# Performance work log

Hardware: AMD Instinct MI355X
Metric: run time of the kernel (lower is better)

## Reference

```python
import jax, jax.numpy as jnp
import numpy as np

EPS = 1e-7      # GENConv message epsilon
BN_EPS = 1e-5   # torch BatchNorm1d eps


def _genconv(x, src, dst, n, w1, b1, gamma, beta, w2, b2):
    # GENConv(aggr='softmax_sg', t=1.0): msg = relu(x_j)+eps, per-feature
    # scatter-softmax weights (stop-grad), weighted sum, residual, MLP
    # [Linear -> BatchNorm(train stats) -> ReLU -> Linear].
    msg = jnp.maximum(x[src], 0.0) + EPS                         # [E, d]
    m = jax.ops.segment_max(msg, dst, num_segments=n)            # [N, d]
    e = jnp.exp(msg - m[dst])
    s = jax.ops.segment_sum(e, dst, num_segments=n)
    alpha = jax.lax.stop_gradient(e / (s[dst] + 1e-16))          # softmax_sg
    agg = jax.ops.segment_sum(msg * alpha, dst, num_segments=n)  # [N, d]
    h = agg + x
    h = h @ w1 + b1
    mu = jnp.mean(h, axis=0)
    var = jnp.var(h, axis=0)
    h = (h - mu) * jax.lax.rsqrt(var + BN_EPS) * gamma + beta
    h = jnp.maximum(h, 0.0)
    return h @ w2 + b2


def _forward(x, edge_index, batch, target,
             g1_w1, g1_b1, g1_g, g1_be, g1_w2, g1_b2,
             g2_w1, g2_b1, g2_g, g2_be, g2_w2, g2_b2,
             g3_w1, g3_b1, g3_g, g3_be, g3_w2, g3_b2,
             fg1_w, fg1_b, fg2_w, fg2_b, fg3_w, fg3_b,
             emb, cw, cb, fxt_w, fxt_b,
             f1_w, f1_b, f2_w, f2_b, o_w, o_b):
    n = x.shape[0]
    nb = target.shape[0]
    src, dst = edge_index[0], edge_index[1]
    h = jnp.maximum(_genconv(x, src, dst, n, g1_w1, g1_b1, g1_g, g1_be, g1_w2, g1_b2), 0.0)
    h = jnp.maximum(_genconv(h, src, dst, n, g2_w1, g2_b1, g2_g, g2_be, g2_w2, g2_b2), 0.0)
    h = jnp.maximum(_genconv(h, src, dst, n, g3_w1, g3_b1, g3_g, g3_be, g3_w2, g3_b2), 0.0)
    # global mean pool over graphs
    sums = jax.ops.segment_sum(h, batch, num_segments=nb)
    cnt = jax.ops.segment_sum(jnp.ones((n, 1), h.dtype), batch, num_segments=nb)
    xg = sums / jnp.maximum(cnt, 1.0)
    xg = jnp.maximum(xg @ fg1_w + fg1_b, 0.0)
    xg = jnp.maximum(xg @ fg2_w + fg2_b, 0.0)
    xg = jnp.maximum(xg @ fg3_w + fg3_b, 0.0)
    # protein branch: embed [B,1000,128], Conv1d(1000->32,k=8) over embed axis
    ext = emb[target]                                            # [B, 1000, 128]
    conv = jax.lax.conv_general_dilated(
        ext, cw, (1,), 'VALID',
        dimension_numbers=('NCW', 'OIW', 'NCW')) + cb[None, :, None]  # [B, 32, 121]
    xt = conv.reshape(nb, 32 * 121) @ fxt_w + fxt_b
    xc = jnp.concatenate([xg, xt], axis=1)                       # [B, 256]
    xc = jnp.maximum(xc @ f1_w + f1_b, 0.0)
    xc = jnp.maximum(xc @ f2_w + f2_b, 0.0)
    return xc @ o_w + o_b


def _lin(k, i, o):
    kw, kb = jax.random.split(k)
    s = 1.0 / np.sqrt(i)
    return (jax.random.uniform(kw, (i, o), jnp.float32, -s, s),
            jax.random.uniform(kb, (o,), jnp.float32, -s, s))


def setup_inputs():
    key = jax.random.key(0)
    ks = jax.random.split(key, 32)
    N, E, B, D = 30000, 150000, 256, 78
    d = {}
    d['x'] = jax.random.normal(ks[0], (N, D), jnp.float32)
    d['edge_index'] = jax.random.randint(ks[1], (2, E), 0, N)
    d['batch'] = jnp.sort(jax.random.randint(ks[2], (N,), 0, B))
    d['target'] = jax.random.randint(ks[3], (B, 1000), 0, 26)
    dims = [(78, 156, 78), (78, 156, 312), (312, 624, 624)]
    for li, (i, hdim, o) in enumerate(dims, start=1):
        w1, b1 = _lin(ks[4 + 2 * li], i, hdim)
        w2, b2 = _lin(ks[5 + 2 * li], hdim, o)
        d['g%d_w1' % li], d['g%d_b1' % li] = w1, b1
        d['g%d_g' % li] = jnp.ones((hdim,), jnp.float32)
        d['g%d_be' % li] = jnp.zeros((hdim,), jnp.float32)
        d['g%d_w2' % li], d['g%d_b2' % li] = w2, b2
    d['fg1_w'], d['fg1_b'] = _lin(ks[14], 624, 512)
    d['fg2_w'], d['fg2_b'] = _lin(ks[15], 512, 1024)
    d['fg3_w'], d['fg3_b'] = _lin(ks[16], 1024, 128)
    d['emb'] = jax.random.normal(ks[17], (26, 128), jnp.float32)
    s = 1.0 / np.sqrt(1000 * 8)
    d['cw'] = jax.random.uniform(ks[18], (32, 1000, 8), jnp.float32, -s, s)
    d['cb'] = jax.random.uniform(ks[19], (32,), jnp.float32, -s, s)
    d['fxt_w'], d['fxt_b'] = _lin(ks[20], 32 * 121, 128)
    d['f1_w'], d['f1_b'] = _lin(ks[21], 256, 1024)
    d['f2_w'], d['f2_b'] = _lin(ks[22], 1024, 512)
    d['o_w'], d['o_b'] = _lin(ks[23], 512, 1)
    return d


def reference(x, edge_index, batch, target,
              g1_w1, g1_b1, g1_g, g1_be, g1_w2, g1_b2,
              g2_w1, g2_b1, g2_g, g2_be, g2_w2, g2_b2,
              g3_w1, g3_b1, g3_g, g3_be, g3_w2, g3_b2,
              fg1_w, fg1_b, fg2_w, fg2_b, fg3_w, fg3_b,
              emb, cw, cb, fxt_w, fxt_b,
              f1_w, f1_b, f2_w, f2_b, o_w, o_b):
    return _forward(x, edge_index, batch, target,
                    g1_w1, g1_b1, g1_g, g1_be, g1_w2, g1_b2,
                    g2_w1, g2_b1, g2_g, g2_be, g2_w2, g2_b2,
                    g3_w1, g3_b1, g3_g, g3_be, g3_w2, g3_b2,
                    fg1_w, fg1_b, fg2_w, fg2_b, fg3_w, fg3_b,
                    emb, cw, cb, fxt_w, fxt_b,
                    f1_w, f1_b, f2_w, f2_b, o_w, o_b)
```

## Files before the change

### kernel.cpp

```cpp
#include <hip/hip_runtime.h>
#include <hip/hip_bf16.h>

typedef unsigned short u16;
typedef __attribute__((ext_vector_type(8))) short bh8;
typedef __attribute__((ext_vector_type(4))) float f32x4;

static __device__ __forceinline__ float b2fu(u16 u) {
    union { float f; unsigned int i; } x;
    x.i = ((unsigned int)u) << 16;
    return x.f;
}
static __device__ __forceinline__ u16 f2bu(float f) {
    __hip_bfloat16 h = __float2bfloat16(f);
    union { __hip_bfloat16 h; u16 u; } x;
    x.h = h;
    return x.u;
}

static __device__ __forceinline__ void gload16(const u16* g, u16* l) {
    __builtin_amdgcn_global_load_lds(
        (const __attribute__((address_space(1))) unsigned int*)(const void*)g,
        (__attribute__((address_space(3))) unsigned int*)(void*)l, 16, 0, 0);
}


__global__ __launch_bounds__(256) void const_out_kernel(float* __restrict__ out, float v, int n) {
    int i = blockIdx.x * 256 + threadIdx.x;
    if (i < n) out[i] = v;
}


__global__ __launch_bounds__(256) void hist2_kernel(const int* __restrict__ dst,
                                                    const int* __restrict__ batch,
                                                    int* __restrict__ hist,
                                                    int* __restrict__ ghist, int E, int N) {
    int i = blockIdx.x * 256 + threadIdx.x;
    if (i < E) atomicAdd(&hist[dst[i]], 1);
    else if (i < E + N) atomicAdd(&ghist[batch[i - E]], 1);
}

__global__ __launch_bounds__(256) void scan_kernel(const int* __restrict__ hist,
                                                   int* __restrict__ rowptr,
                                                   int* __restrict__ fill, int N) {
    __shared__ int csum[256];
    __shared__ int coff[257];
    int t = threadIdx.x;
    int chunk = (N + 255) / 256;
    int lo = min(t * chunk, N), hi = min(lo + chunk, N);
    int s = 0;
    for (int i = lo; i < hi; i++) s += hist[i];
    csum[t] = s;
    __syncthreads();
    if (t == 0) {
        int acc = 0;
        for (int i = 0; i < 256; i++) { coff[i] = acc; acc += csum[i]; }
        rowptr[N] = acc;
    }
    __syncthreads();
    int run = coff[t];
    for (int i = lo; i < hi; i++) {
        rowptr[i] = run;
        fill[i] = run;
        run += hist[i];
    }
}

__global__ __launch_bounds__(256) void scan_tiles(const int* __restrict__ hist, int N,
                                                  int* __restrict__ rowptr,
                                                  int* __restrict__ tsum) {
    int tid = threadIdx.x;
    int i = blockIdx.x * 256 + tid;
    int v = (i < N) ? hist[i] : 0;
    __shared__ int s[256];
    s[tid] = v;
    __syncthreads();
    for (int off = 1; off < 256; off <<= 1) {
        int t = (tid >= off) ? s[tid - off] : 0;
        __syncthreads();
        s[tid] += t;
        __syncthreads();
    }
    if (i < N) rowptr[i] = s[tid] - v;
    if (tid == 255) tsum[blockIdx.x] = s[255];
}

__global__ __launch_bounds__(256) void scan_tsum(const int* __restrict__ tsum, int ntiles,
                                                 int* __restrict__ toff,
                                                 int* __restrict__ totalp) {
    int tid = threadIdx.x;
    int v = (tid < ntiles) ? tsum[tid] : 0;
    __shared__ int s[256];
    s[tid] = v;
    __syncthreads();
    for (int off = 1; off < 256; off <<= 1) {
        int t = (tid >= off) ? s[tid - off] : 0;
        __syncthreads();
        s[tid] += t;
        __syncthreads();
    }
    if (tid < ntiles) toff[tid] = s[tid] - v;
    if (tid == 255) *totalp = s[255];
}

__global__ __launch_bounds__(256) void scan_apply(int* __restrict__ rowptr,
                                                  const int* __restrict__ toff, int N,
                                                  int* __restrict__ fill) {
    int i = blockIdx.x * 256 + threadIdx.x;
    if (i < N) {
        int r = rowptr[i] + toff[blockIdx.x];
        rowptr[i] = r;
        fill[i] = r;
    }
}

__global__ __launch_bounds__(256) void scatter_kernel(const int* __restrict__ src,
                                                      const int* __restrict__ dst,
                                                      int* __restrict__ fill,
                                                      int* __restrict__ srcs, int E) {
    int e = blockIdx.x * 256 + threadIdx.x;
    if (e < E) {
        int p = atomicAdd(&fill[dst[e]], 1);
        srcs[p] = src[e];
    }
}


template <typename T, int VEC>
__global__ __launch_bounds__(256) void agg_kernel(const T* __restrict__ x,
                                                  const int* __restrict__ rowptr,
                                                  const int* __restrict__ srcs,
                                                  u16* __restrict__ out, int d, int ldx,
                                                  int Kp, int N) {
    int n = blockIdx.y * 4 + (threadIdx.x >> 6);
    int f0 = (blockIdx.x * 64 + (threadIdx.x & 63)) * VEC;
    if (n >= N || f0 >= Kp) return;
    size_t o = (size_t)n * Kp + f0;
    if (f0 >= d) {
#pragma unroll
        for (int i = 0; i < VEC; i++) out[o + i] = 0;
        return;
    }
    auto loadV = [&](const T* row, float* v) {
        if constexpr (sizeof(T) == 4) {
            float2 t = *reinterpret_cast<const float2*>(row);
            v[0] = t.x; v[1] = t.y;
        } else if constexpr (VEC == 2) {
            unsigned int u = *reinterpret_cast<const unsigned int*>(row);
            v[0] = b2fu((u16)(u & 0xffff)); v[1] = b2fu((u16)(u >> 16));
        } else if constexpr (VEC == 4) {
            uint2 u = *reinterpret_cast<const uint2*>(row);
            v[0] = b2fu((u16)(u.x & 0xffff)); v[1] = b2fu((u16)(u.x >> 16));
            v[2] = b2fu((u16)(u.y & 0xffff)); v[3] = b2fu((u16)(u.y >> 16));
        } else {
            uint4 u = *reinterpret_cast<const uint4*>(row);
            v[0] = b2fu((u16)(u.x & 0xffff)); v[1] = b2fu((u16)(u.x >> 16));
            v[2] = b2fu((u16)(u.y & 0xffff)); v[3] = b2fu((u16)(u.y >> 16));
            v[4] = b2fu((u16)(u.z & 0xffff)); v[5] = b2fu((u16)(u.z >> 16));
            v[6] = b2fu((u16)(u.w & 0xffff)); v[7] = b2fu((u16)(u.w >> 16));
        }
    };
    int e0 = rowptr[n], e1 = rowptr[n + 1];
    float s[VEC] = {}, t[VEC] = {};
    for (int e = e0; e < e1; e++) {
        int sr = srcs[e];
        float v[VEC];
        loadV(x + (size_t)sr * ldx + f0, v);
#pragma unroll
        for (int i = 0; i < VEC; i++) {
            float m = fmaxf(v[i], 0.f) + 1e-7f;
            float wv = __expf(m);
            s[i] += wv;
            t[i] += m * wv;
        }
    }
    float xs[VEC];
    loadV(x + (size_t)n * ldx + f0, xs);
    u16 ob[VEC];
#pragma unroll
    for (int i = 0; i < VEC; i++) {
        float a = t[i] / (s[i] + 1e-16f) + xs[i];
        ob[i] = (f0 + i < d) ? f2bu(a) : (u16)0;
    }
    if constexpr (VEC == 2) {
        *reinterpret_cast<unsigned int*>(out + o) =
            (unsigned int)ob[0] | ((unsigned int)ob[1] << 16);
    } else if constexpr (VEC == 4) {
        uint2 u;
        u.x = (unsigned int)ob[0] | ((unsigned int)ob[1] << 16);
        u.y = (unsigned int)ob[2] | ((unsigned int)ob[3] << 16);
        *reinterpret_cast<uint2*>(out + o) = u;
    } else {
        uint4 u;
        u.x = (unsigned int)ob[0] | ((unsigned int)ob[1] << 16);
        u.y = (unsigned int)ob[2] | ((unsigned int)ob[3] << 16);
        u.z = (unsigned int)ob[4] | ((unsigned int)ob[5] << 16);
        u.w = (unsigned int)ob[6] | ((unsigned int)ob[7] << 16);
        *reinterpret_cast<uint4*>(out + o) = u;
    }
}


struct WtJobs {
    const float* W[6];
    u16* WT[6];
    int K[6], N[6], Kp[6], Np[6];
};

__global__ __launch_bounds__(256) void wt_cvt6(WtJobs jb) {
    int jz = blockIdx.z;
    int Kp = jb.Kp[jz], Np = jb.Np[jz];
    int n = blockIdx.y * 4 + (threadIdx.x >> 6);
    int k = blockIdx.x * 64 + (threadIdx.x & 63);
    if (n >= Np || k >= Kp) return;
    int K = jb.K[jz], N = jb.N[jz];
    float v = (n < N && k < K) ? jb.W[jz][(size_t)k * N + n] : 0.f;
    jb.WT[jz][(size_t)n * Kp + k] = f2bu(v);
}


template <int AMODE, int EMODE, bool RELU, typename CT>
__global__ __launch_bounds__(256) void gemm_mfma(const u16* __restrict__ A,
                                                 const u16* __restrict__ BT,
                                                 const float* __restrict__ bias,
                                                 CT* __restrict__ C, int ldc, int M, int Ncols,
                                                 int Kp, int kLen, int nbx, int nby, int spx,
                                                 const float* __restrict__ scale,
                                                 const float* __restrict__ shift,
                                                 float* __restrict__ osum,
                                                 float* __restrict__ osumsq) {
    int xcd = blockIdx.x & 7;
    int j = blockIdx.x >> 3;
    int bx = j % nbx;
    int by = xcd * spx + j / nbx;
    if (by >= nby) return;
    __shared__ u16 As[2][128 * 32];
    __shared__ u16 Bs[2][128 * 32];
    const int tid = threadIdx.x;
    const int lane = tid & 63;
    const int w = tid >> 6;
    const int bm = by * 128;
    const int bn = bx * 128;
    const int kw = blockIdx.y * kLen;
    f32x4 acc[4][4] = {};

    const int r0 = w * 16 + (lane >> 2);
    const int r1 = r0 + 64;
    const int sw = ((lane & 3) ^ ((r0 >> 1) & 3)) << 3;
    const u16* Ag0 = A + (size_t)(bm + r0) * Kp + sw + kw;
    const u16* Ag1 = A + (size_t)(bm + r1) * Kp + sw + kw;
    const u16* Bg0 = BT + (size_t)(bn + r0) * Kp + sw + kw;
    const u16* Bg1 = BT + (size_t)(bn + r1) * Kp + sw + kw;
    const int wb = w << 9;

    uint4 a0r, a1r;
    auto stageB = [&](int b, int koff) {
        gload16(Bg0 + koff, &Bs[b][wb]);
        gload16(Bg1 + koff, &Bs[b][2048 + wb]);
    };
    auto stageA_lds = [&](int b, int koff) {
        gload16(Ag0 + koff, &As[b][wb]);
        gload16(Ag1 + koff, &As[b][2048 + wb]);
    };
    auto loadA_reg = [&](int koff) {
        a0r = *reinterpret_cast<const uint4*>(Ag0 + koff);
        a1r = *reinterpret_cast<const uint4*>(Ag1 + koff);
    };
    auto writeA_reg = [&](int b, int koff) {
        int f0 = sw + kw + koff;
        float4 sc0 = *reinterpret_cast<const float4*>(scale + f0);
        float4 sc1 = *reinterpret_cast<const float4*>(scale + f0 + 4);
        float4 sh0 = *reinterpret_cast<const float4*>(shift + f0);
        float4 sh1 = *reinterpret_cast<const float4*>(shift + f0 + 4);
        auto tf2 = [](unsigned int u, float sa, float sb, float ha, float hb) {
            float h0 = b2fu((u16)(u & 0xffff)), h1 = b2fu((u16)(u >> 16));
            float v0 = fmaxf(fmaf(h0, sa, ha), 0.f);
            float v1 = fmaxf(fmaf(h1, sb, hb), 0.f);
            return (unsigned int)f2bu(v0) | ((unsigned int)f2bu(v1) << 16);
        };
        uint4 o0, o1;
        o0.x = tf2(a0r.x, sc0.x, sc0.y, sh0.x, sh0.y);
        o0.y = tf2(a0r.y, sc0.z, sc0.w, sh0.z, sh0.w);
        o0.z = tf2(a0r.z, sc1.x, sc1.y, sh1.x, sh1.y);
        o0.w = tf2(a0r.w, sc1.z, sc1.w, sh1.z, sh1.w);
        o1.x = tf2(a1r.x, sc0.x, sc0.y, sh0.x, sh0.y);
        o1.y = tf2(a1r.y, sc0.z, sc0.w, sh0.z, sh0.w);
        o1.z = tf2(a1r.z, sc1.x, sc1.y, sh1.x, sh1.y);
        o1.w = tf2(a1r.w, sc1.z, sc1.w, sh1.z, sh1.w);
        *reinterpret_cast<uint4*>(&As[b][wb + lane * 8]) = o0;
        *reinterpret_cast<uint4*>(&As[b][2048 + wb + lane * 8]) = o1;
    };

    const int fm = (w >> 1) * 64 + (lane & 15);
    const int fn = (w & 1) * 64 + (lane & 15);
    const int g = lane >> 4;
    const int ka = (g ^ ((fm >> 1) & 3)) << 3;
    const int kb = (g ^ ((fn >> 1) & 3)) << 3;

    const int nk = kLen >> 5;
    if constexpr (AMODE == 0) {
        stageA_lds(0, 0);
        stageB(0, 0);
        asm volatile("s_waitcnt vmcnt(0)" ::: "memory");
    } else {
        loadA_reg(0);
        stageB(0, 0);
        asm volatile("s_waitcnt vmcnt(0)" ::: "memory");
        writeA_reg(0, 0);
        asm volatile("s_waitcnt lgkmcnt(0)" ::: "memory");
    }
    __builtin_amdgcn_s_barrier();
    for (int k = 0; k < nk; k++) {
        const int cur = k & 1;
        if (k + 1 < nk) {
            if constexpr (AMODE == 0) stageA_lds(cur ^ 1, (k + 1) << 5);
            else loadA_reg((k + 1) << 5);
            stageB(cur ^ 1, (k + 1) << 5);
        }
        bh8 af[4], bf[4];
#pragma unroll
        for (int mt = 0; mt < 4; mt++)
            af[mt] = *reinterpret_cast<const bh8*>(&As[cur][(fm + mt * 16) * 32 + ka]);
#pragma unroll
        for (int nt = 0; nt < 4; nt++)
            bf[nt] = *reinterpret_cast<const bh8*>(&Bs[cur][(fn + nt * 16) * 32 + kb]);
        asm volatile("s_waitcnt lgkmcnt(0)" ::: "memory");
        __builtin_amdgcn_sched_barrier(0);
        __builtin_amdgcn_s_setprio(1);
#pragma unroll
        for (int mt = 0; mt < 4; mt++)
#pragma unroll
            for (int nt = 0; nt < 4; nt++)
                acc[mt][nt] = __builtin_amdgcn_mfma_f32_16x16x32_bf16(af[mt], bf[nt],
                                                                      acc[mt][nt], 0, 0, 0);
        __builtin_amdgcn_s_setprio(0);
        __builtin_amdgcn_sched_barrier(0);
        asm volatile("s_waitcnt vmcnt(0)" ::: "memory");
        if constexpr (AMODE == 1) {
            __builtin_amdgcn_sched_barrier(0);
            if (k + 1 < nk) writeA_reg(cur ^ 1, (k + 1) << 5);
            asm volatile("s_waitcnt lgkmcnt(0)" ::: "memory");
        }
        __builtin_amdgcn_s_barrier();
    }
    const int rq = (lane >> 4) * 4;
    const int cl = lane & 15;
    if constexpr (EMODE == 0) {
#pragma unroll
        for (int mt = 0; mt < 4; mt++) {
#pragma unroll
            for (int nt = 0; nt < 4; nt++) {
                int n = bn + (w & 1) * 64 + nt * 16 + cl;
                if (n >= ldc) continue;
                bool valid = (n < Ncols);
                float bv = valid ? bias[n] : 0.f;
#pragma unroll
                for (int r = 0; r < 4; r++) {
                    int m = bm + (w >> 1) * 64 + mt * 16 + rq + r;
                    if (m >= M) continue;
                    float v = valid ? acc[mt][nt][r] + bv : 0.f;
                    if (RELU) v = fmaxf(v, 0.f);
                    if (sizeof(CT) == 2)
                        C[(size_t)m * ldc + n] = (CT)f2bu(v);
                    else
                        C[(size_t)m * ldc + n] = (CT)v;
                }
            }
        }
    } else if constexpr (EMODE == 1) {
        float cs[4] = {0.f, 0.f, 0.f, 0.f}, cq[4] = {0.f, 0.f, 0.f, 0.f};
#pragma unroll
        for (int nt = 0; nt < 4; nt++) {
            int n = bn + (w & 1) * 64 + nt * 16 + cl;
            if (n >= ldc) continue;
            float bv = (n < Ncols) ? bias[n] : 0.f;
#pragma unroll
            for (int mt = 0; mt < 4; mt++) {
#pragma unroll
                for (int r = 0; r < 4; r++) {
                    int m = bm + (w >> 1) * 64 + mt * 16 + rq + r;
                    if (m >= M) continue;
                    float v = (n < Ncols) ? acc[mt][nt][r] + bv : 0.f;
                    C[(size_t)m * ldc + n] = (CT)f2bu(v);
                    cs[nt] += v;
                    cq[nt] += v * v;
                }
            }
        }
        float* red = (float*)&As[0][0];
        const int slot = (w >> 1) * 4 + (lane >> 4);
#pragma unroll
        for (int nt = 0; nt < 4; nt++) {
            int nl = (w & 1) * 64 + nt * 16 + cl;
            red[nl * 8 + slot] = cs[nt];
            red[1024 + nl * 8 + slot] = cq[nt];
        }
        __syncthreads();
        if (tid < 128) {
            int n = bn + tid;
            if (n < Ncols) {
                float s = 0.f, q = 0.f;
#pragma unroll
                for (int i = 0; i < 8; i++) {
                    s += red[tid * 8 + i];
                    q += red[1024 + tid * 8 + i];
                }
                atomicAdd(&osum[n], s);
                atomicAdd(&osumsq[n], q);
            }
        }
    } else {
#pragma unroll
        for (int mt = 0; mt < 4; mt++) {
#pragma unroll
            for (int nt = 0; nt < 4; nt++) {
                int n = bn + (w & 1) * 64 + nt * 16 + cl;
                if (n >= Ncols) continue;
#pragma unroll
                for (int r = 0; r < 4; r++) {
                    int m = bm + (w >> 1) * 64 + mt * 16 + rq + r;
                    if (m >= M) continue;
                    atomicAdd((float*)&C[(size_t)m * ldc + n], acc[mt][nt][r]);
                }
            }
        }
    }
}


__global__ __launch_bounds__(256) void bn_final(const float* __restrict__ sum,
                                                const float* __restrict__ sumsq,
                                                const float* __restrict__ gamma,
                                                const float* __restrict__ beta,
                                                float* __restrict__ scale,
                                                float* __restrict__ shift, int dh, int Kp,
                                                float invN) {
    int i = blockIdx.x * 256 + threadIdx.x;
    if (i >= Kp) return;
    if (i < dh) {
        float mu = sum[i] * invN;
        float var = sumsq[i] * invN - mu * mu;
        float sc = gamma[i] / sqrtf(var + 1e-5f);
        scale[i] = sc;
        shift[i] = beta[i] - mu * sc;
    } else {
        scale[i] = 0.f;
        shift[i] = 0.f;
    }
}


__global__ __launch_bounds__(256) void pool_seg(const u16* __restrict__ h,
                                                const int* __restrict__ goff,
                                                float* __restrict__ gsum, int d) {
    int g = blockIdx.y;
    int c = threadIdx.x & 63;
    int f = blockIdx.x * 64 + c;
    int wv = threadIdx.x >> 6;
    int r0 = goff[g], r1 = goff[g + 1];
    float s = 0.f;
    if (f < d)
        for (int r = r0 + wv; r < r1; r += 4) s += b2fu(h[(size_t)r * d + f]);
    __shared__ float ls[4][64];
    ls[wv][c] = s;
    __syncthreads();
    if (wv == 0 && f < d) {
        float tot = ls[0][c] + ls[1][c] + ls[2][c] + ls[3][c];
        gsum[(size_t)g * d + f] = tot / fmaxf((float)(r1 - r0), 1.f);
    }
}


__global__ __launch_bounds__(256) void gemm_sk(const float* __restrict__ A, int lda,
                                               const float* __restrict__ B, int ldb,
                                               float* __restrict__ C, int ldc, int M, int K,
                                               int Nn, int KC, int klim) {
    __shared__ float As[16][17];
    __shared__ float Bs[16][68];
    const int tid = threadIdx.x;
    const int bn = blockIdx.x * 64;
    const int bm = blockIdx.y * 16;
    const int k0 = blockIdx.z * KC;
    const int kend = min(K, k0 + KC);
    const int tx = tid & 63;
    const int ty = tid >> 6;
    float acc[4] = {};
    const int am = bm + (tid >> 4);
    const int ak = tid & 15;
    for (int kk0 = k0; kk0 < kend; kk0 += 16) {
        {
            int k = kk0 + ak;
            float v = (am < M && k < kend) ? A[(size_t)am * lda + k] : 0.f;
            if (k < klim) v = fmaxf(v, 0.f);
            As[ak][tid >> 4] = v;
        }
#pragma unroll
        for (int i = 0; i < 4; i++) {
            int k = kk0 + ty + 4 * i;
            Bs[ty + 4 * i][tx] = (k < kend && bn + tx < Nn) ? B[(size_t)k * ldb + bn + tx] : 0.f;
        }
        __syncthreads();
#pragma unroll
        for (int kk = 0; kk < 16; kk++) {
            float b = Bs[kk][tx];
#pragma unroll
            for (int i = 0; i < 4; i++) acc[i] = fmaf(As[kk][ty + 4 * i], b, acc[i]);
        }
        __syncthreads();
    }
    if (bn + tx < Nn) {
#pragma unroll
        for (int i = 0; i < 4; i++) {
            int m = bm + ty + 4 * i;
            if (m < M) atomicAdd(&C[(size_t)m * ldc + bn + tx], acc[i]);
        }
    }
}

static void launch_gemm_small(const float* A, int lda, const float* B, int ldb,
                              float* C, int ldc, int M, int K, int Nn, int klim,
                              hipStream_t stream) {
    int gx = (Nn + 63) / 64, gy = (M + 15) / 16;
    int tiles = gx * gy;
    int ksplit = 512 / tiles;
    if (ksplit < 1) ksplit = 1;
    int maxsplit = (K + 63) / 64;
    if (ksplit > maxsplit) ksplit = maxsplit;
    int KC = (((K + ksplit - 1) / ksplit) + 15) & ~15;
    ksplit = (K + KC - 1) / KC;
    gemm_sk<<<dim3(gx, gy, ksplit), 256, 0, stream>>>(A, lda, B, ldb, C, ldc, M, K, Nn, KC,
                                                      klim);
}


struct FillJobs {
    float* C[6];
    const float* b[6];
    int ld[6], n0[6], n1[6];
};

__global__ __launch_bounds__(256) void prefill6(FillJobs jb, int M) {
    int jz = blockIdx.z;
    int w = jb.n1[jz] - jb.n0[jz];
    int i = blockIdx.x * 256 + threadIdx.x;
    if (i >= M * w) return;
    int m = i / w, n = i - m * w;
    jb.C[jz][(size_t)m * jb.ld[jz] + jb.n0[jz] + n] = jb.b[jz][n];
}


__global__ __launch_bounds__(256) void hone_kernel(const int* __restrict__ target,
                                                   u16* __restrict__ H, int total) {
    int i = blockIdx.x * 256 + threadIdx.x;
    if (i >= total) return;
    int b = i / 1000, pos = i - b * 1000;
    int t = target[i];
    H[((size_t)b * 26 + t) * 1024 + pos] = 0x3F80;
}

__global__ __launch_bounds__(256) void cwt_cvt(const float* __restrict__ cw,
                                               u16* __restrict__ BT) {
    int n = blockIdx.y;
    int kk = blockIdx.x * 256 + threadIdx.x;
    int o = n >> 3, k = n & 7;
    float v = (kk < 1000) ? cw[(size_t)o * 8000 + (size_t)kk * 8 + k] : 0.f;
    BT[(size_t)n * 1024 + kk] = f2bu(v);
}

__global__ __launch_bounds__(256) void prot_conv_kernel(const float* __restrict__ S,
                                                        const float* __restrict__ emb,
                                                        const float* __restrict__ cb,
                                                        float* __restrict__ out) {
    int b = blockIdx.x;
    int tid = threadIdx.x;
    __shared__ float Sl[6656];
    __shared__ float el[26 * 128];
    for (int i = tid; i < 6656; i += 256) Sl[i] = S[(size_t)b * 6656 + i];
    for (int i = tid; i < 26 * 128; i += 256) el[i] = emb[i];
    __syncthreads();
    for (int j = tid; j < 3872; j += 256) {
        int o = j / 121;
        int w = j - o * 121;
        float acc = cb[o];
        for (int t = 0; t < 26; t++) {
#pragma unroll
            for (int k = 0; k < 8; k++)
                acc = fmaf(Sl[t * 256 + o * 8 + k], el[t * 128 + w + k], acc);
        }
        out[(size_t)b * 3872 + j] = acc;
    }
}


__global__ __launch_bounds__(256) void out_kernel(const float* __restrict__ A,
                                                  const float* __restrict__ w,
                                                  const float* __restrict__ bias,
                                                  float* __restrict__ out, int M, int K) {
    int wave = threadIdx.x >> 6;
    int lane = threadIdx.x & 63;
    int r = blockIdx.x * 4 + wave;
    if (r >= M) return;
    float acc = 0.f;
    for (int k = lane; k < K; k += 64) acc += fmaxf(A[(size_t)r * K + k], 0.f) * w[k];
    for (int off = 32; off > 0; off >>= 1) acc += __shfl_down(acc, off, 64);
    if (lane == 0) out[r] = acc + bias[0];
}


static inline int KP(int k) { return (k + 31) & ~31; }
static inline int NP(int n) { return (n + 127) & ~127; }
static inline int LD8(int n) { return (n + 7) & ~7; }

extern "C" void kernel_launch(void* const* d_in, const int* in_sizes, int n_in, void* d_out,
                              int out_size, void* d_ws, size_t ws_size, hipStream_t stream) {
    static const int exp_sizes[39] = {
        2340000, 300000, 30000, 256000,
        12168, 156, 156, 156, 12168, 78,
        12168, 156, 156, 156, 48672, 312,
        194688, 624, 624, 624, 389376, 624,
        319488, 512, 524288, 1024, 131072, 128,
        3328, 256000, 32, 495616, 128,
        262144, 1024, 524288, 512, 512, 1};
    int bad = (n_in != 39) ? 100 : -1;
    if (bad < 0)
        for (int i = 0; i < 39; i++)
            if (in_sizes[i] != exp_sizes[i]) { bad = i; break; }
    if (bad >= 0) {
        const_out_kernel<<<1, 256, 0, stream>>>((float*)d_out, 2048.f + 8.f * bad, out_size);
        return;
    }

    const int N = 30000, E = 150000, B = 256;
    const int Mp = 30080;
    const int nby = 235, spx = 30;
    const int ntiles = (N + 255) / 256;
    const float* x_in = (const float*)d_in[0];
    const int* ei = (const int*)d_in[1];
    const int* src = ei;
    const int* dst = ei + E;
    const int* batch = (const int*)d_in[2];
    const int* target = (const int*)d_in[3];

    char* p = (char*)d_ws;
    auto carve = [&](size_t bytes) {
        char* r = p;
        p += (bytes + 15) & ~(size_t)15;
        return r;
    };
    int* hist = (int*)carve((size_t)(N + B) * 4);
    int* ghist = hist + N;
    int* rowptr = (int*)carve((size_t)(N + 1) * 4);
    int* fill = (int*)carve((size_t)N * 4);
    int* srcs = (int*)carve((size_t)E * 4);
    int* goff = (int*)carve((size_t)(B + 1) * 4);
    int* gfill = (int*)carve((size_t)B * 4);
    int* tsum = (int*)carve(256 * 4);
    int* toff = (int*)carve(256 * 4);
    float* sum_ = (float*)carve(2 * 624 * 4);
    float* sumsq_ = sum_ + 624;
    float* scale_ = (float*)carve(640 * 4);
    float* shift_ = (float*)carve(640 * 4);
    float* zero256 = (float*)carve(256 * 4);
    float* gsum = (float*)carve((size_t)B * 624 * 4);
    float* fc1 = (float*)carve((size_t)B * 512 * 4);
    float* fc2 = (float*)carve((size_t)B * 1024 * 4);
    float* xc = (float*)carve((size_t)B * 256 * 4);
    float* fcc1 = (float*)carve((size_t)B * 1024 * 4);
    float* fcc2 = (float*)carve((size_t)B * 512 * 4);
    float* Sbuf = (float*)carve((size_t)B * 6656 * 4);
    float* convb = (float*)carve((size_t)B * 3872 * 4);
    u16* Hbuf = (u16*)carve((size_t)B * 26 * 1024 * 2);
    u16* cwT = (u16*)carve((size_t)256 * 1024 * 2);
    u16* Abf = (u16*)carve((size_t)Mp * 640 * 2);
    u16* hmidb = (u16*)carve((size_t)Mp * 640 * 2);
    u16* Lout = (u16*)carve((size_t)N * 624 * 2);
    struct Layer { int di, dh, dn, w1, b1, g, be, w2, b2; };
    const Layer L[3] = {
        {78, 156, 78, 4, 5, 6, 7, 8, 9},
        {78, 156, 312, 10, 11, 12, 13, 14, 15},
        {312, 624, 624, 16, 17, 18, 19, 20, 21},
    };
    u16* WT1[3];
    u16* WT2[3];
    for (int li = 0; li < 3; li++) {
        WT1[li] = (u16*)carve((size_t)NP(L[li].dh) * KP(L[li].di) * 2);
        WT2[li] = (u16*)carve((size_t)NP(L[li].dn) * KP(L[li].dh) * 2);
    }
    size_t need = (size_t)(p - (char*)d_ws);
    if (ws_size < need) {
        const_out_kernel<<<1, 256, 0, stream>>>((float*)d_out,
                                                1024.f + (float)(ws_size >> 20), out_size);
        return;
    }

    hipMemsetAsync(hist, 0, (size_t)(N + B) * 4, stream);
    hipMemsetAsync(zero256, 0, 256 * 4, stream);
    hist2_kernel<<<(E + N + 255) / 256, 256, 0, stream>>>(dst, batch, hist, ghist, E, N);
    scan_tiles<<<ntiles, 256, 0, stream>>>(hist, N, rowptr, tsum);
    scan_tsum<<<1, 256, 0, stream>>>(tsum, ntiles, toff, rowptr + N);
    scan_apply<<<ntiles, 256, 0, stream>>>(rowptr, toff, N, fill);
    scan_kernel<<<1, 256, 0, stream>>>(ghist, goff, gfill, B);
    scatter_kernel<<<(E + 255) / 256, 256, 0, stream>>>(src, dst, fill, srcs, E);

    {
        WtJobs jb;
        int mgx = 1, mgy = 1;
        for (int li = 0; li < 3; li++) {
            jb.W[2 * li] = (const float*)d_in[L[li].w1];
            jb.WT[2 * li] = WT1[li];
            jb.K[2 * li] = L[li].di; jb.N[2 * li] = L[li].dh;
            jb.Kp[2 * li] = KP(L[li].di); jb.Np[2 * li] = NP(L[li].dh);
            jb.W[2 * li + 1] = (const float*)d_in[L[li].w2];
            jb.WT[2 * li + 1] = WT2[li];
            jb.K[2 * li + 1] = L[li].dh; jb.N[2 * li + 1] = L[li].dn;
            jb.Kp[2 * li + 1] = KP(L[li].dh); jb.Np[2 * li + 1] = NP(L[li].dn);
        }
        for (int i = 0; i < 6; i++) {
            int gx = (jb.Kp[i] + 63) / 64, gy = jb.Np[i] / 4;
            if (gx > mgx) mgx = gx;
            if (gy > mgy) mgy = gy;
        }
        wt_cvt6<<<dim3(mgx, mgy, 6), 256, 0, stream>>>(jb);
    }

    const int ldo[3] = {LD8(L[0].dn), LD8(L[1].dn), LD8(L[2].dn)};
    for (int li = 0; li < 3; li++) {
        const int di = L[li].di, dh = L[li].dh, dn = L[li].dn;
        const int Kp1 = KP(di), Kp2 = KP(dh);
        if (li == 0)
            agg_kernel<float, 2><<<dim3((Kp1 / 2 + 63) / 64, (N + 3) / 4), 256, 0, stream>>>(
                x_in, rowptr, srcs, Abf, di, di, Kp1, N);
        else if (li == 1)
            agg_kernel<u16, 4><<<dim3((Kp1 / 4 + 63) / 64, (N + 3) / 4), 256, 0, stream>>>(
                Lout, rowptr, srcs, Abf, di, ldo[0], Kp1, N);
        else
            agg_kernel<u16, 8><<<dim3((Kp1 / 8 + 63) / 64, (N + 3) / 4), 256, 0, stream>>>(
                Lout, rowptr, srcs, Abf, di, ldo[1], Kp1, N);
        hipMemsetAsync(sum_, 0, 2 * 624 * 4, stream);
        {
            int nbx = NP(dh) / 128;
            gemm_mfma<0, 1, false, u16><<<dim3(8 * spx * nbx), 256, 0, stream>>>(
                Abf, WT1[li], (const float*)d_in[L[li].b1], hmidb, Kp2, N, dh, Kp1, Kp1, nbx,
                nby, spx, nullptr, nullptr, sum_, sumsq_);
        }
        bn_final<<<(Kp2 + 255) / 256, 256, 0, stream>>>(
            sum_, sumsq_, (const float*)d_in[L[li].g], (const float*)d_in[L[li].be], scale_,
            shift_, dh, Kp2, 1.0f / N);
        {
            int nbx = NP(dn) / 128;
            gemm_mfma<1, 0, true, u16><<<dim3(8 * spx * nbx), 256, 0, stream>>>(
                hmidb, WT2[li], (const float*)d_in[L[li].b2], Lout, ldo[li], N, dn, Kp2, Kp2,
                nbx, nby, spx, scale_, shift_, nullptr, nullptr);
        }
    }

    pool_seg<<<dim3(10, B), 256, 0, stream>>>(Lout, goff, gsum, 624);

    {
        FillJobs fj;
        fj.C[0] = fc1;  fj.b[0] = (const float*)d_in[23]; fj.ld[0] = 512;  fj.n0[0] = 0;   fj.n1[0] = 512;
        fj.C[1] = fc2;  fj.b[1] = (const float*)d_in[25]; fj.ld[1] = 1024; fj.n0[1] = 0;   fj.n1[1] = 1024;
        fj.C[2] = xc;   fj.b[2] = (const float*)d_in[27]; fj.ld[2] = 256;  fj.n0[2] = 0;   fj.n1[2] = 128;
        fj.C[3] = xc;   fj.b[3] = (const float*)d_in[32]; fj.ld[3] = 256;  fj.n0[3] = 128; fj.n1[3] = 256;
        fj.C[4] = fcc1; fj.b[4] = (const float*)d_in[34]; fj.ld[4] = 1024; fj.n0[4] = 0;   fj.n1[4] = 1024;
        fj.C[5] = fcc2; fj.b[5] = (const float*)d_in[36]; fj.ld[5] = 512;  fj.n0[5] = 0;   fj.n1[5] = 512;
        prefill6<<<dim3((B * 1024 + 255) / 256, 1, 6), 256, 0, stream>>>(fj, B);
    }

    launch_gemm_small(gsum, 624, (const float*)d_in[22], 512, fc1, 512, B, 624, 512, 0, stream);
    launch_gemm_small(fc1, 512, (const float*)d_in[24], 1024, fc2, 1024, B, 512, 1024, 512,
                      stream);
    launch_gemm_small(fc2, 1024, (const float*)d_in[26], 128, xc, 256, B, 1024, 128, 1024,
                      stream);

    hipMemsetAsync(Hbuf, 0, (size_t)B * 26 * 1024 * 2, stream);
    hipMemsetAsync(Sbuf, 0, (size_t)B * 6656 * 4, stream);
    hone_kernel<<<(B * 1000 + 255) / 256, 256, 0, stream>>>(target, Hbuf, B * 1000);
    cwt_cvt<<<dim3(4, 256), 256, 0, stream>>>((const float*)d_in[29], cwT);
    {
        int nbxS = 2, nbyS = 52, spxS = 7;
        gemm_mfma<0, 2, false, float><<<dim3(8 * spxS * nbxS, 4), 256, 0, stream>>>(
            Hbuf, cwT, zero256, Sbuf, 256, 6656, 256, 1024, 256, nbxS, nbyS, spxS, nullptr,
            nullptr, nullptr, nullptr);
    }
    prot_conv_kernel<<<B, 256, 0, stream>>>(Sbuf, (const float*)d_in[28],
                                            (const float*)d_in[30], convb);
    launch_gemm_small(convb, 3872, (const float*)d_in[31], 128, xc + 128, 256, B, 3872, 128, 0,
                      stream);

    launch_gemm_small(xc, 256, (const float*)d_in[33], 1024, fcc1, 1024, B, 256, 1024, 128,
                      stream);
    launch_gemm_small(fcc1, 1024, (const float*)d_in[35], 512, fcc2, 512, B, 1024, 512, 1024,
                      stream);
    out_kernel<<<(B + 3) / 4, 256, 0, stream>>>(fcc2, (const float*)d_in[37],
                                                (const float*)d_in[38], (float*)d_out, B, 512);
}
```

Before: 772.2 us.

## Fuse protein branch into one kernel, fold BN finalize into GEMM, merge scans

The protein branch (one-hot buffer, weight transpose, split-K MFMA GEMM with atomics, conv kernel, fxt linear) is replaced by a single per-sample kernel. It accumulates conv weights per token class in LDS, does the 26-class conv, and applies the fxt projection directly. The BatchNorm finalize kernel is folded into the second GEMM's prologue, which computes scale and shift into shared memory. The per-layer memsets and the separate graph-offset scan are merged into one memset and a two-block scan kernel. This cuts launches and intermediate buffers, but the protein work now runs on scalar FMA with one block per sample and serialized LDS accumulation over 1000 positions.

```diff
diff --git a/kernel.cpp b/kernel.cpp
--- a/kernel.cpp
+++ b/kernel.cpp
@@ -37,32 +37,6 @@
     int i = blockIdx.x * 256 + threadIdx.x;
     if (i < E) atomicAdd(&hist[dst[i]], 1);
     else if (i < E + N) atomicAdd(&ghist[batch[i - E]], 1);
-}
-
-__global__ __launch_bounds__(256) void scan_kernel(const int* __restrict__ hist,
-                                                   int* __restrict__ rowptr,
-                                                   int* __restrict__ fill, int N) {
-    __shared__ int csum[256];
-    __shared__ int coff[257];
-    int t = threadIdx.x;
-    int chunk = (N + 255) / 256;
-    int lo = min(t * chunk, N), hi = min(lo + chunk, N);
-    int s = 0;
-    for (int i = lo; i < hi; i++) s += hist[i];
-    csum[t] = s;
-    __syncthreads();
-    if (t == 0) {
-        int acc = 0;
-        for (int i = 0; i < 256; i++) { coff[i] = acc; acc += csum[i]; }
-        rowptr[N] = acc;
-    }
-    __syncthreads();
-    int run = coff[t];
-    for (int i = lo; i < hi; i++) {
-        rowptr[i] = run;
-        fill[i] = run;
-        run += hist[i];
-    }
 }
 
 __global__ __launch_bounds__(256) void scan_tiles(const int* __restrict__ hist, int N,
@@ -84,22 +58,43 @@
     if (tid == 255) tsum[blockIdx.x] = s[255];
 }
 
-__global__ __launch_bounds__(256) void scan_tsum(const int* __restrict__ tsum, int ntiles,
+__global__ __launch_bounds__(256) void scan_misc(const int* __restrict__ tsum, int ntiles,
                                                  int* __restrict__ toff,
-                                                 int* __restrict__ totalp) {
+                                                 int* __restrict__ totalp,
+                                                 const int* __restrict__ ghist,
+                                                 int* __restrict__ goff,
+                                                 int* __restrict__ gfill, int B) {
     int tid = threadIdx.x;
-    int v = (tid < ntiles) ? tsum[tid] : 0;
-    __shared__ int s[256];
-    s[tid] = v;
-    __syncthreads();
-    for (int off = 1; off < 256; off <<= 1) {
-        int t = (tid >= off) ? s[tid - off] : 0;
-        __syncthreads();
-        s[tid] += t;
-        __syncthreads();
-    }
-    if (tid < ntiles) toff[tid] = s[tid] - v;
-    if (tid == 255) *totalp = s[255];
+    if (blockIdx.x == 0) {
+        int v = (tid < ntiles) ? tsum[tid] : 0;
+        __shared__ int s[256];
+        s[tid] = v;
+        __syncthreads();
+        for (int off = 1; off < 256; off <<= 1) {
+            int t = (tid >= off) ? s[tid - off] : 0;
+            __syncthreads();
+            s[tid] += t;
+            __syncthreads();
+        }
+        if (tid < ntiles) toff[tid] = s[tid] - v;
+        if (tid == 255) *totalp = s[255];
+    } else {
+        int v = (tid < B) ? ghist[tid] : 0;
+        __shared__ int s2[256];
+        s2[tid] = v;
+        __syncthreads();
+        for (int off = 1; off < 256; off <<= 1) {
+            int t = (tid >= off) ? s2[tid - off] : 0;
+            __syncthreads();
+            s2[tid] += t;
+            __syncthreads();
+        }
+        if (tid < B) {
+            goff[tid] = s2[tid] - v;
+            gfill[tid] = s2[tid] - v;
+        }
+        if (tid == 255) goff[B] = s2[255];
+    }
 }
 
 __global__ __launch_bounds__(256) void scan_apply(int* __restrict__ rowptr,
@@ -223,9 +218,12 @@
                                                  const u16* __restrict__ BT,
                                                  const float* __restrict__ bias,
                                                  CT* __restrict__ C, int ldc, int M, int Ncols,
-                                                 int Kp, int kLen, int nbx, int nby, int spx,
-                                                 const float* __restrict__ scale,
-                                                 const float* __restrict__ shift,
+                                                 int Kp, int nbx, int nby, int spx,
+                                                 const float* __restrict__ bnsum,
+                                                 const float* __restrict__ bnsumsq,
+                                                 const float* __restrict__ gamma,
+                                                 const float* __restrict__ beta,
+                                                 float invN, int dhBN,
                                                  float* __restrict__ osum,
                                                  float* __restrict__ osumsq) {
     int xcd = blockIdx.x & 7;
@@ -235,21 +233,37 @@
     if (by >= nby) return;
     __shared__ u16 As[2][128 * 32];
     __shared__ u16 Bs[2][128 * 32];
+    __shared__ float scl[AMODE == 1 ? 640 : 1];
+    __shared__ float shf[AMODE == 1 ? 640 : 1];
     const int tid = threadIdx.x;
     const int lane = tid & 63;
     const int w = tid >> 6;
     const int bm = by * 128;
     const int bn = bx * 128;
-    const int kw = blockIdx.y * kLen;
     f32x4 acc[4][4] = {};
+
+    if constexpr (AMODE == 1) {
+        for (int i = tid; i < Kp; i += 256) {
+            float sc = 0.f, sh = 0.f;
+            if (i < dhBN) {
+                float mu = bnsum[i] * invN;
+                float var = bnsumsq[i] * invN - mu * mu;
+                sc = gamma[i] / sqrtf(var + 1e-5f);
+                sh = beta[i] - mu * sc;
+            }
+            scl[i] = sc;
+            shf[i] = sh;
+        }
+        __syncthreads();
+    }
 
     const int r0 = w * 16 + (lane >> 2);
     const int r1 = r0 + 64;
     const int sw = ((lane & 3) ^ ((r0 >> 1) & 3)) << 3;
-    const u16* Ag0 = A + (size_t)(bm + r0) * Kp + sw + kw;
-    const u16* Ag1 = A + (size_t)(bm + r1) * Kp + sw + kw;
-    const u16* Bg0 = BT + (size_t)(bn + r0) * Kp + sw + kw;
-    const u16* Bg1 = BT + (size_t)(bn + r1) * Kp + sw + kw;
+    const u16* Ag0 = A + (size_t)(bm + r0) * Kp + sw;
+    const u16* Ag1 = A + (size_t)(bm + r1) * Kp + sw;
+    const u16* Bg0 = BT + (size_t)(bn + r0) * Kp + sw;
+    const u16* Bg1 = BT + (size_t)(bn + r1) * Kp + sw;
     const int wb = w << 9;
 
     uint4 a0r, a1r;
@@ -266,11 +280,11 @@
         a1r = *reinterpret_cast<const uint4*>(Ag1 + koff);
     };
     auto writeA_reg = [&](int b, int koff) {
-        int f0 = sw + kw + koff;
-        float4 sc0 = *reinterpret_cast<const float4*>(scale + f0);
-        float4 sc1 = *reinterpret_cast<const float4*>(scale + f0 + 4);
-        float4 sh0 = *reinterpret_cast<const float4*>(shift + f0);
-        float4 sh1 = *reinterpret_cast<const float4*>(shift + f0 + 4);
+        int f0 = sw + koff;
+        float4 sc0 = *reinterpret_cast<const float4*>(&scl[f0]);
+        float4 sc1 = *reinterpret_cast<const float4*>(&scl[f0 + 4]);
+        float4 sh0 = *reinterpret_cast<const float4*>(&shf[f0]);
+        float4 sh1 = *reinterpret_cast<const float4*>(&shf[f0 + 4]);
         auto tf2 = [](unsigned int u, float sa, float sb, float ha, float hb) {
             float h0 = b2fu((u16)(u & 0xffff)), h1 = b2fu((u16)(u >> 16));
             float v0 = fmaxf(fmaf(h0, sa, ha), 0.f);
@@ -296,7 +310,7 @@
     const int ka = (g ^ ((fm >> 1) & 3)) << 3;
     const int kb = (g ^ ((fn >> 1) & 3)) << 3;
 
-    const int nk = kLen >> 5;
+    const int nk = Kp >> 5;
     if constexpr (AMODE == 0) {
         stageA_lds(0, 0);
         stageB(0, 0);
@@ -366,7 +380,7 @@
                 }
             }
         }
-    } else if constexpr (EMODE == 1) {
+    } else {
         float cs[4] = {0.f, 0.f, 0.f, 0.f}, cq[4] = {0.f, 0.f, 0.f, 0.f};
 #pragma unroll
         for (int nt = 0; nt < 4; nt++) {
@@ -408,43 +422,6 @@
                 atomicAdd(&osumsq[n], q);
             }
         }
-    } else {
-#pragma unroll
-        for (int mt = 0; mt < 4; mt++) {
-#pragma unroll
-            for (int nt = 0; nt < 4; nt++) {
-                int n = bn + (w & 1) * 64 + nt * 16 + cl;
-                if (n >= Ncols) continue;
-#pragma unroll
-                for (int r = 0; r < 4; r++) {
-                    int m = bm + (w >> 1) * 64 + mt * 16 + rq + r;
-                    if (m >= M) continue;
-                    atomicAdd((float*)&C[(size_t)m * ldc + n], acc[mt][nt][r]);
-                }
-            }
-        }
-    }
-}
-
-
-__global__ __launch_bounds__(256) void bn_final(const float* __restrict__ sum,
-                                                const float* __restrict__ sumsq,
-                                                const float* __restrict__ gamma,
-                                                const float* __restrict__ beta,
-                                                float* __restrict__ scale,
-                                                float* __restrict__ shift, int dh, int Kp,
-                                                float invN) {
-    int i = blockIdx.x * 256 + threadIdx.x;
-    if (i >= Kp) return;
-    if (i < dh) {
-        float mu = sum[i] * invN;
-        float var = sumsq[i] * invN - mu * mu;
-        float sc = gamma[i] / sqrtf(var + 1e-5f);
-        scale[i] = sc;
-        shift[i] = beta[i] - mu * sc;
-    } else {
-        scale[i] = 0.f;
-        shift[i] = 0.f;
     }
 }
 
@@ -548,45 +525,53 @@
 }
 
 
-__global__ __launch_bounds__(256) void hone_kernel(const int* __restrict__ target,
-                                                   u16* __restrict__ H, int total) {
-    int i = blockIdx.x * 256 + threadIdx.x;
-    if (i >= total) return;
-    int b = i / 1000, pos = i - b * 1000;
-    int t = target[i];
-    H[((size_t)b * 26 + t) * 1024 + pos] = 0x3F80;
-}
-
-__global__ __launch_bounds__(256) void cwt_cvt(const float* __restrict__ cw,
-                                               u16* __restrict__ BT) {
-    int n = blockIdx.y;
-    int kk = blockIdx.x * 256 + threadIdx.x;
-    int o = n >> 3, k = n & 7;
-    float v = (kk < 1000) ? cw[(size_t)o * 8000 + (size_t)kk * 8 + k] : 0.f;
-    BT[(size_t)n * 1024 + kk] = f2bu(v);
-}
-
-__global__ __launch_bounds__(256) void prot_conv_kernel(const float* __restrict__ S,
-                                                        const float* __restrict__ emb,
-                                                        const float* __restrict__ cb,
-                                                        float* __restrict__ out) {
+__global__ __launch_bounds__(256) void prot_fused(const int* __restrict__ target,
+                                                  const float* __restrict__ cw,
+                                                  const float* __restrict__ emb,
+                                                  const float* __restrict__ cb,
+                                                  const float* __restrict__ fxtw,
+                                                  const float* __restrict__ fxtb,
+                                                  float* __restrict__ xc) {
     int b = blockIdx.x;
     int tid = threadIdx.x;
-    __shared__ float Sl[6656];
+    __shared__ float Sl[26 * 256];
     __shared__ float el[26 * 128];
-    for (int i = tid; i < 6656; i += 256) Sl[i] = S[(size_t)b * 6656 + i];
+    __shared__ int tl[1000];
+    __shared__ float cv[3872];
+    __shared__ float xs[128];
+    for (int i = tid; i < 26 * 256; i += 256) Sl[i] = 0.f;
     for (int i = tid; i < 26 * 128; i += 256) el[i] = emb[i];
+    for (int i = tid; i < 1000; i += 256) tl[i] = target[(size_t)b * 1000 + i];
+    __syncthreads();
+    {
+        int o = tid >> 3, k = tid & 7;
+        const float* cwp = cw + (size_t)o * 8000 + k;
+        for (int i = 0; i < 1000; i++) {
+            int t = tl[i];
+            Sl[t * 256 + tid] += cwp[(size_t)i * 8];
+        }
+    }
     __syncthreads();
     for (int j = tid; j < 3872; j += 256) {
         int o = j / 121;
         int w = j - o * 121;
         float acc = cb[o];
-        for (int t = 0; t < 26; t++) {
+        for (int t = 0; t < 26; t++)
 #pragma unroll
             for (int k = 0; k < 8; k++)
                 acc = fmaf(Sl[t * 256 + o * 8 + k], el[t * 128 + w + k], acc);
-        }
-        out[(size_t)b * 3872 + j] = acc;
+        cv[j] = acc;
+    }
+    __syncthreads();
+    {
+        int n = tid & 127, half = tid >> 7;
+        float acc = 0.f;
+        int j0 = half * 1936, j1 = j0 + 1936;
+#pragma unroll 4
+        for (int j = j0; j < j1; j++) acc = fmaf(cv[j], fxtw[(size_t)j * 128 + n], acc);
+        if (half == 1) xs[n] = acc;
+        __syncthreads();
+        if (half == 0) xc[(size_t)b * 256 + 128 + n] = acc + xs[n] + fxtb[n];
     }
 }
 
@@ -646,8 +631,10 @@
         p += (bytes + 15) & ~(size_t)15;
         return r;
     };
-    int* hist = (int*)carve((size_t)(N + B) * 4);
+    int* hist = (int*)carve((size_t)(N + B) * 4 + 3 * 1280 * 4);
     int* ghist = hist + N;
+    float* sums = (float*)(hist + N + B);
+    const size_t zero_bytes = (size_t)(N + B) * 4 + 3 * 1280 * 4;
     int* rowptr = (int*)carve((size_t)(N + 1) * 4);
     int* fill = (int*)carve((size_t)N * 4);
     int* srcs = (int*)carve((size_t)E * 4);
@@ -655,21 +642,12 @@
     int* gfill = (int*)carve((size_t)B * 4);
     int* tsum = (int*)carve(256 * 4);
     int* toff = (int*)carve(256 * 4);
-    float* sum_ = (float*)carve(2 * 624 * 4);
-    float* sumsq_ = sum_ + 624;
-    float* scale_ = (float*)carve(640 * 4);
-    float* shift_ = (float*)carve(640 * 4);
-    float* zero256 = (float*)carve(256 * 4);
     float* gsum = (float*)carve((size_t)B * 624 * 4);
     float* fc1 = (float*)carve((size_t)B * 512 * 4);
     float* fc2 = (float*)carve((size_t)B * 1024 * 4);
     float* xc = (float*)carve((size_t)B * 256 * 4);
     float* fcc1 = (float*)carve((size_t)B * 1024 * 4);
     float* fcc2 = (float*)carve((size_t)B * 512 * 4);
-    float* Sbuf = (float*)carve((size_t)B * 6656 * 4);
-    float* convb = (float*)carve((size_t)B * 3872 * 4);
-    u16* Hbuf = (u16*)carve((size_t)B * 26 * 1024 * 2);
-    u16* cwT = (u16*)carve((size_t)256 * 1024 * 2);
     u16* Abf = (u16*)carve((size_t)Mp * 640 * 2);
     u16* hmidb = (u16*)carve((size_t)Mp * 640 * 2);
     u16* Lout = (u16*)carve((size_t)N * 624 * 2);
@@ -692,13 +670,11 @@
         return;
     }
 
-    hipMemsetAsync(hist, 0, (size_t)(N + B) * 4, stream);
-    hipMemsetAsync(zero256, 0, 256 * 4, stream);
+    hipMemsetAsync(hist, 0, zero_bytes, stream);
     hist2_kernel<<<(E + N + 255) / 256, 256, 0, stream>>>(dst, batch, hist, ghist, E, N);
     scan_tiles<<<ntiles, 256, 0, stream>>>(hist, N, rowptr, tsum);
-    scan_tsum<<<1, 256, 0, stream>>>(tsum, ntiles, toff, rowptr + N);
+    scan_misc<<<2, 256, 0, stream>>>(tsum, ntiles, toff, rowptr + N, ghist, goff, gfill, B);
     scan_apply<<<ntiles, 256, 0, stream>>>(rowptr, toff, N, fill);
-    scan_kernel<<<1, 256, 0, stream>>>(ghist, goff, gfill, B);
     scatter_kernel<<<(E + 255) / 256, 256, 0, stream>>>(src, dst, fill, srcs, E);
 
     {
@@ -726,6 +702,8 @@
     for (int li = 0; li < 3; li++) {
         const int di = L[li].di, dh = L[li].dh, dn = L[li].dn;
         const int Kp1 = KP(di), Kp2 = KP(dh);
+        float* sumL = sums + li * 1280;
+        float* sumsqL = sumL + 640;
         if (li == 0)
             agg_kernel<float, 2><<<dim3((Kp1 / 2 + 63) / 64, (N + 3) / 4), 256, 0, stream>>>(
                 x_in, rowptr, srcs, Abf, di, di, Kp1, N);
@@ -735,21 +713,18 @@
         else
             agg_kernel<u16, 8><<<dim3((Kp1 / 8 + 63) / 64, (N + 3) / 4), 256, 0, stream>>>(
                 Lout, rowptr, srcs, Abf, di, ldo[1], Kp1, N);
-        hipMemsetAsync(sum_, 0, 2 * 624 * 4, stream);
         {
             int nbx = NP(dh) / 128;
             gemm_mfma<0, 1, false, u16><<<dim3(8 * spx * nbx), 256, 0, stream>>>(
-                Abf, WT1[li], (const float*)d_in[L[li].b1], hmidb, Kp2, N, dh, Kp1, Kp1, nbx,
-                nby, spx, nullptr, nullptr, sum_, sumsq_);
-        }
-        bn_final<<<(Kp2 + 255) / 256, 256, 0, stream>>>(
-            sum_, sumsq_, (const float*)d_in[L[li].g], (const float*)d_in[L[li].be], scale_,
-            shift_, dh, Kp2, 1.0f / N);
+                Abf, WT1[li], (const float*)d_in[L[li].b1], hmidb, Kp2, N, dh, Kp1, nbx, nby,
+                spx, nullptr, nullptr, nullptr, nullptr, 0.f, 0, sumL, sumsqL);
+        }
         {
             int nbx = NP(dn) / 128;
             gemm_mfma<1, 0, true, u16><<<dim3(8 * spx * nbx), 256, 0, stream>>>(
-                hmidb, WT2[li], (const float*)d_in[L[li].b2], Lout, ldo[li], N, dn, Kp2, Kp2,
-                nbx, nby, spx, scale_, shift_, nullptr, nullptr);
+                hmidb, WT2[li], (const float*)d_in[L[li].b2], Lout, ldo[li], N, dn, Kp2, nbx,
+                nby, spx, sumL, sumsqL, (const float*)d_in[L[li].g],
+                (const float*)d_in[L[li].be], 1.0f / N, dh, nullptr, nullptr);
         }
     }
 
@@ -757,34 +732,23 @@
 
     {
         FillJobs fj;
-        fj.C[0] = fc1;  fj.b[0] = (const float*)d_in[23]; fj.ld[0] = 512;  fj.n0[0] = 0;   fj.n1[0] = 512;
-        fj.C[1] = fc2;  fj.b[1] = (const float*)d_in[25]; fj.ld[1] = 1024; fj.n0[1] = 0;   fj.n1[1] = 1024;
-        fj.C[2] = xc;   fj.b[2] = (const float*)d_in[27]; fj.ld[2] = 256;  fj.n0[2] = 0;   fj.n1[2] = 128;
-        fj.C[3] = xc;   fj.b[3] = (const float*)d_in[32]; fj.ld[3] = 256;  fj.n0[3] = 128; fj.n1[3] = 256;
-        fj.C[4] = fcc1; fj.b[4] = (const float*)d_in[34]; fj.ld[4] = 1024; fj.n0[4] = 0;   fj.n1[4] = 1024;
-        fj.C[5] = fcc2; fj.b[5] = (const float*)d_in[36]; fj.ld[5] = 512;  fj.n0[5] = 0;   fj.n1[5] = 512;
-        prefill6<<<dim3((B * 1024 + 255) / 256, 1, 6), 256, 0, stream>>>(fj, B);
-    }
+        fj.C[0] = fc1;  fj.b[0] = (const float*)d_in[23]; fj.ld[0] = 512;  fj.n0[0] = 0; fj.n1[0] = 512;
+        fj.C[1] = fc2;  fj.b[1] = (const float*)d_in[25]; fj.ld[1] = 1024; fj.n0[1] = 0; fj.n1[1] = 1024;
+        fj.C[2] = xc;   fj.b[2] = (const float*)d_in[27]; fj.ld[2] = 256;  fj.n0[2] = 0; fj.n1[2] = 128;
+        fj.C[3] = fcc1; fj.b[3] = (const float*)d_in[34]; fj.ld[3] = 1024; fj.n0[3] = 0; fj.n1[3] = 1024;
+        fj.C[4] = fcc2; fj.b[4] = (const float*)d_in[36]; fj.ld[4] = 512;  fj.n0[4] = 0; fj.n1[4] = 512;
+        fj.C[5] = nullptr; fj.b[5] = nullptr; fj.ld[5] = 0; fj.n0[5] = 0; fj.n1[5] = 0;
+        prefill6<<<dim3((B * 1024 + 255) / 256, 1, 5), 256, 0, stream>>>(fj, B);
+    }
+
+    prot_fused<<<B, 256, 0, stream>>>(target, (const float*)d_in[29], (const float*)d_in[28],
+                                      (const float*)d_in[30], (const float*)d_in[31],
+                                      (const float*)d_in[32], xc);
 
     launch_gemm_small(gsum, 624, (const float*)d_in[22], 512, fc1, 512, B, 624, 512, 0, stream);
     launch_gemm_small(fc1, 512, (const float*)d_in[24], 1024, fc2, 1024, B, 512, 1024, 512,
                       stream);
     launch_gemm_small(fc2, 1024, (const float*)d_in[26], 128, xc, 256, B, 1024, 128, 1024,
-                      stream);
-
-    hipMemsetAsync(Hbuf, 0, (size_t)B * 26 * 1024 * 2, stream);
-    hipMemsetAsync(Sbuf, 0, (size_t)B * 6656 * 4, stream);
-    hone_kernel<<<(B * 1000 + 255) / 256, 256, 0, stream>>>(target, Hbuf, B * 1000);
-    cwt_cvt<<<dim3(4, 256), 256, 0, stream>>>((const float*)d_in[29], cwT);
-    {
-        int nbxS = 2, nbyS = 52, spxS = 7;
-        gemm_mfma<0, 2, false, float><<<dim3(8 * spxS * nbxS, 4), 256, 0, stream>>>(
-            Hbuf, cwT, zero256, Sbuf, 256, 6656, 256, 1024, 256, nbxS, nbyS, spxS, nullptr,
-            nullptr, nullptr, nullptr);
-    }
-    prot_conv_kernel<<<B, 256, 0, stream>>>(Sbuf, (const float*)d_in[28],
-                                            (const float*)d_in[30], convb);
-    launch_gemm_small(convb, 3872, (const float*)d_in[31], 128, xc + 128, 256, B, 3872, 128, 0,
                       stream);
 
     launch_gemm_small(xc, 256, (const float*)d_in[33], 1024, fcc1, 1024, B, 256, 1024, 128,
```

Measured after the change: 848.8 us. 9.9% more time.
